# Optimization experiments

Hardware: AMD Instinct MI355X
Metric: run time of the kernel (lower is better)

The kernel has to match this reference:

```python
import jax, jax.numpy as jnp
import numpy as np

NH = 32          # num_attention_heads
LAYER_ID = 3     # per-layer scaling coeff = LAYER_ID + 1
SQ, B, H = 1024, 2, 4096
MEM_LEN = 1024
HD = H // NH


def setup_inputs() -> dict:
    key = jax.random.key(0)
    ks = jax.random.split(key, 6)
    hidden_states = jax.random.normal(ks[0], (SQ, B, H), dtype=jnp.float32)
    mem = jax.random.normal(ks[1], (B, MEM_LEN, 2 * NH * HD), dtype=jnp.float32) * 0.5
    qkv_w = jax.random.normal(ks[2], (3 * H, H), dtype=jnp.float32) * 0.02
    qkv_b = jax.random.normal(ks[3], (3 * H,), dtype=jnp.float32) * 0.02
    dense_w = jax.random.normal(ks[4], (H, H), dtype=jnp.float32) * 0.02
    dense_b = jax.random.normal(ks[5], (H,), dtype=jnp.float32) * 0.02
    # causal mask over new tokens; mem positions fully visible. True = masked.
    kv = MEM_LEN + SQ
    mask = ((jnp.arange(kv)[None, :] - MEM_LEN) > jnp.arange(SQ)[:, None])
    mask = mask[None, None, :, :]  # [1,1,sq,kv]
    # position ids of new tokens continue after the mem cache: [b, sq]
    position_ids = jnp.broadcast_to(MEM_LEN + jnp.arange(SQ, dtype=jnp.int64), (B, SQ))
    return {"hidden_states": hidden_states, "mask": mask, "position_ids": position_ids,
            "mem": mem, "qkv_w": qkv_w, "qkv_b": qkv_b, "dense_w": dense_w, "dense_b": dense_b}


def _rotate_half(x):
    x1, x2 = jnp.split(x, 2, axis=-1)
    return jnp.concatenate((-x2, x1), axis=-1)


def _rotary_tables(max_pos):
    inv_freq = 1.0 / (10000.0 ** (jnp.arange(0, HD, 2, dtype=jnp.float32) / HD))
    t = jnp.arange(max_pos, dtype=jnp.float32)
    freqs = jnp.einsum('i,j->ij', t, inv_freq)          # [L, HD/2]
    emb = jnp.concatenate((freqs, freqs), axis=-1)      # [L, HD]
    return jnp.cos(emb), jnp.sin(emb)


def reference(hidden_states, mask, position_ids, mem, qkv_w, qkv_b, dense_w, dense_b):
    sq, b, h = hidden_states.shape
    coeff = float(LAYER_ID + 1)
    # QKV projection: [sq,b,3H] -> [sq,b,nh,3*hd] -> split
    mixed = jnp.einsum('sbh,oh->sbo', hidden_states, qkv_w) + qkv_b
    mixed = mixed.reshape(sq, b, NH, 3 * HD)
    q, k, v = jnp.split(mixed, 3, axis=-1)              # each [sq,b,nh,hd]
    # rotary embedding with position indices (position_ids: [b,sq] -> [sq,b])
    pos = position_ids.T                                 # [sq,b]
    cos_t, sin_t = _rotary_tables(MEM_LEN + SQ)          # table up to max pos + 1
    cos = cos_t[pos][:, :, None, :]                      # [sq,b,1,hd]
    sin = sin_t[pos][:, :, None, :]
    q = q * cos + _rotate_half(q) * sin
    k = k * cos + _rotate_half(k) * sin
    # mem-KV concat: mem [b, mem_len, 2*nh*hd] -> memk/memv [mem_len,b,nh,hd]
    m = mem.reshape(b, MEM_LEN, 2, NH, HD).transpose(2, 1, 0, 3, 4)
    k = jnp.concatenate((m[0], k), axis=0)               # [kv,b,nh,hd]
    v = jnp.concatenate((m[1], v), axis=0)
    # per-layer scaled attention scores
    q = q / (np.sqrt(HD) * coeff)
    scores = jnp.einsum('sbnh,tbnh->bnst', q, k)         # [b,nh,sq,kv]
    scores = jnp.where(mask, -10000.0, scores)
    scores = scores * coeff
    probs = jax.nn.softmax(scores, axis=-1)
    ctx = jnp.einsum('bnst,tbnh->sbnh', probs, v).reshape(sq, b, h)
    out = jnp.einsum('sbh,oh->sbo', ctx, dense_w) + dense_b
    return out
```

## Files before the change

kernel.cpp:

```cpp
#include <hip/hip_runtime.h>


typedef __attribute__((ext_vector_type(4))) float f32x4;
typedef __attribute__((ext_vector_type(8))) short bf16x8;
typedef unsigned short u16;

#define SQ   1024
#define BSZ  2
#define H    4096
#define NH   32
#define HD   128
#define MEML 1024
#define KV   2048

__device__ __forceinline__ u16 f32_to_bf16(float f) {
  union { float f; unsigned int u; } v; v.f = f;
  unsigned int r = v.u + 0x7FFFu + ((v.u >> 16) & 1u);
  return (u16)(r >> 16);
}
__device__ __forceinline__ float bf16_to_f32(u16 x) {
  union { unsigned int u; float f; } v; v.u = ((unsigned int)x) << 16; return v.f;
}

__device__ __forceinline__ void gload_lds16(const void* g, void* l) {
  __builtin_amdgcn_global_load_lds((const __attribute__((address_space(1))) void*)g,
                                   (__attribute__((address_space(3))) void*)l, 16, 0, 0);
}

__global__ __launch_bounds__(256) void conv_bf16(const float* __restrict__ in,
                                                 u16* __restrict__ out, int n4) {
  int idx = blockIdx.x * 256 + threadIdx.x;
  if (idx < n4) {
    float4 v = ((const float4*)in)[idx];
    ushort4 o;
    o.x = f32_to_bf16(v.x); o.y = f32_to_bf16(v.y);
    o.z = f32_to_bf16(v.z); o.w = f32_to_bf16(v.w);
    ((ushort4*)out)[idx] = o;
  }
}

__global__ __launch_bounds__(256) void rope_tables(float* __restrict__ cost, float* __restrict__ sint) {
  int idx = blockIdx.x * 256 + threadIdx.x;
  int s = idx >> 6, j = idx & 63;
  float inv = powf(10000.0f, -(float)j / 64.0f);
  float ang = (float)(MEML + s) * inv;
  cost[idx] = cosf(ang);
  sint[idx] = sinf(ang);
}

__global__ __launch_bounds__(512, 2) void gemm3p(const u16* __restrict__ A, const u16* __restrict__ B,
                                                 const float* __restrict__ bias, u16* __restrict__ C,
                                                 int N, int K) {
  __shared__ char lds[2][57344];
  const int tid = threadIdx.x;
  const int lane = tid & 63;
  const int w = tid >> 6;
  const int wm = w >> 2, wn = w & 3;
  const int rl = lane & 15, cg = lane >> 4;
  const int m0 = blockIdx.y * 256, n0 = blockIdx.x * 192;
  const int nt = K >> 6;

  const int srow = tid >> 3;
  const int scb = ((tid & 7) << 4) ^ ((srow & 7) << 4);

  auto stage_a = [&](int tile, int ua) {
    if (tile >= nt) return;
    gload_lds16((const char*)(A + (size_t)(m0 + ua * 64 + srow) * K + (size_t)tile * 64) + scb,
                lds[tile & 1] + ua * 8192 + tid * 16);
  };
  auto stage_b = [&](int tile, int ub) {
    if (tile >= nt) return;
    gload_lds16((const char*)(B + (size_t)(n0 + ub * 64 + srow) * K + (size_t)tile * 64) + scb,
                lds[tile & 1] + 32768 + ub * 8192 + tid * 16);
  };

  f32x4 acc[8][3];
#pragma unroll
  for (int i = 0; i < 8; ++i)
#pragma unroll
    for (int j = 0; j < 3; ++j) acc[i][j] = (f32x4){0.f, 0.f, 0.f, 0.f};

  bf16x8 af0[4][2], af1[4][2], bf[3][2];

  auto read_am = [&](const char* buf, int mh, bf16x8 (&dst)[4][2]) {
#pragma unroll
    for (int mi = 0; mi < 4; ++mi) {
      int R = wm * 128 + mh * 64 + mi * 16 + rl;
#pragma unroll
      for (int kk = 0; kk < 2; ++kk) {
        int cb = (kk * 64 + cg * 16) ^ ((R & 7) << 4);
        dst[mi][kk] = *(const bf16x8*)(buf + R * 128 + cb);
      }
    }
  };
  auto read_b1 = [&](const char* buf, int nl) {
    int R = wn * 48 + nl * 16 + rl;
#pragma unroll
    for (int kk = 0; kk < 2; ++kk) {
      int cb = (kk * 64 + cg * 16) ^ ((R & 7) << 4);
      bf[nl][kk] = *(const bf16x8*)(buf + 32768 + R * 128 + cb);
    }
  };

#pragma unroll
  for (int u = 0; u < 4; ++u) stage_a(0, u);
#pragma unroll
  for (int u = 0; u < 3; ++u) stage_b(0, u);
#pragma unroll
  for (int u = 0; u < 3; ++u) stage_b(1, u);
  asm volatile("s_waitcnt vmcnt(3)" ::: "memory");
  __builtin_amdgcn_s_barrier();

  for (int kt = 0; kt < nt; ++kt) {
    const char* buf = lds[kt & 1];
    read_am(buf, 0, af0);
    read_b1(buf, 0); read_b1(buf, 1);
    stage_a(kt + 1, 0); stage_a(kt + 1, 1);
    __builtin_amdgcn_s_barrier();
    asm volatile("s_waitcnt lgkmcnt(0)" ::: "memory");
    __builtin_amdgcn_s_setprio(1);
#pragma unroll
    for (int kk = 0; kk < 2; ++kk)
#pragma unroll
      for (int mi = 0; mi < 4; ++mi) {
        acc[mi][0] = __builtin_amdgcn_mfma_f32_16x16x32_bf16(af0[mi][kk], bf[0][kk], acc[mi][0], 0, 0, 0);
        acc[mi][1] = __builtin_amdgcn_mfma_f32_16x16x32_bf16(af0[mi][kk], bf[1][kk], acc[mi][1], 0, 0, 0);
      }
    __builtin_amdgcn_s_setprio(0);
    __builtin_amdgcn_s_barrier();
    read_am(buf, 1, af1);
    read_b1(buf, 2);
    stage_a(kt + 1, 2); stage_a(kt + 1, 3);
    __builtin_amdgcn_s_barrier();
    asm volatile("s_waitcnt lgkmcnt(0)" ::: "memory");
    __builtin_amdgcn_s_setprio(1);
#pragma unroll
    for (int kk = 0; kk < 2; ++kk)
#pragma unroll
      for (int mi = 0; mi < 4; ++mi) {
        acc[4 + mi][1] = __builtin_amdgcn_mfma_f32_16x16x32_bf16(af1[mi][kk], bf[1][kk], acc[4 + mi][1], 0, 0, 0);
        acc[4 + mi][2] = __builtin_amdgcn_mfma_f32_16x16x32_bf16(af1[mi][kk], bf[2][kk], acc[4 + mi][2], 0, 0, 0);
      }
    __builtin_amdgcn_s_setprio(0);
    __builtin_amdgcn_s_barrier();
    stage_b(kt + 2, 0); stage_b(kt + 2, 1); stage_b(kt + 2, 2);
    __builtin_amdgcn_s_barrier();
    __builtin_amdgcn_s_setprio(1);
#pragma unroll
    for (int kk = 0; kk < 2; ++kk)
#pragma unroll
      for (int mi = 0; mi < 4; ++mi) {
        acc[mi][2] = __builtin_amdgcn_mfma_f32_16x16x32_bf16(af0[mi][kk], bf[2][kk], acc[mi][2], 0, 0, 0);
        acc[4 + mi][0] = __builtin_amdgcn_mfma_f32_16x16x32_bf16(af1[mi][kk], bf[0][kk], acc[4 + mi][0], 0, 0, 0);
      }
    __builtin_amdgcn_s_setprio(0);
    if (kt + 2 < nt)      { asm volatile("s_waitcnt vmcnt(3)" ::: "memory"); }
    else if (kt + 1 < nt) { asm volatile("s_waitcnt vmcnt(0)" ::: "memory"); }
    __builtin_amdgcn_s_barrier();
  }

#pragma unroll
  for (int ni = 0; ni < 3; ++ni) {
    int col = n0 + wn * 48 + ni * 16 + rl;
    float bv = bias[col];
#pragma unroll
    for (int mi = 0; mi < 8; ++mi) {
      int rbase = m0 + wm * 128 + mi * 16 + cg * 4;
#pragma unroll
      for (int j = 0; j < 4; ++j)
        C[(size_t)(rbase + j) * N + col] = f32_to_bf16(acc[mi][ni][j] + bv);
    }
  }
}

__global__ __launch_bounds__(512, 2) void gemm2p(const u16* __restrict__ A, const u16* __restrict__ B,
                                                 const float* __restrict__ bias, float* __restrict__ C,
                                                 int N, int K) {
  __shared__ char lds[2][49152];
  const int tid = threadIdx.x;
  const int lane = tid & 63;
  const int w = tid >> 6;
  const int wm = w >> 2, wn = w & 3;
  const int rl = lane & 15, cg = lane >> 4;
  const int m0 = blockIdx.y * 256, n0 = blockIdx.x * 128;
  const int nt = K >> 6;

  const int srow = tid >> 3;
  const int scb = ((tid & 7) << 4) ^ ((srow & 7) << 4);

  auto stage_a = [&](int tile, int ua) {
    if (tile >= nt) return;
    gload_lds16((const char*)(A + (size_t)(m0 + ua * 64 + srow) * K + (size_t)tile * 64) + scb,
                lds[tile & 1] + ua * 8192 + tid * 16);
  };
  auto stage_b = [&](int tile, int ub) {
    if (tile >= nt) return;
    gload_lds16((const char*)(B + (size_t)(n0 + ub * 64 + srow) * K + (size_t)tile * 64) + scb,
                lds[tile & 1] + 32768 + ub * 8192 + tid * 16);
  };

  f32x4 acc[8][2];
#pragma unroll
  for (int i = 0; i < 8; ++i)
#pragma unroll
    for (int j = 0; j < 2; ++j) acc[i][j] = (f32x4){0.f, 0.f, 0.f, 0.f};

  bf16x8 af0[4][2], af1[4][2], bf[2][2];

  auto read_am = [&](const char* buf, int mh, bf16x8 (&dst)[4][2]) {
#pragma unroll
    for (int mi = 0; mi < 4; ++mi) {
      int R = wm * 128 + mh * 64 + mi * 16 + rl;
#pragma unroll
      for (int kk = 0; kk < 2; ++kk) {
        int cb = (kk * 64 + cg * 16) ^ ((R & 7) << 4);
        dst[mi][kk] = *(const bf16x8*)(buf + R * 128 + cb);
      }
    }
  };
  auto read_b1 = [&](const char* buf, int nl) {
    int R = wn * 32 + nl * 16 + rl;
#pragma unroll
    for (int kk = 0; kk < 2; ++kk) {
      int cb = (kk * 64 + cg * 16) ^ ((R & 7) << 4);
      bf[nl][kk] = *(const bf16x8*)(buf + 32768 + R * 128 + cb);
    }
  };

#pragma unroll
  for (int u = 0; u < 4; ++u) stage_a(0, u);
  stage_b(0, 0); stage_b(0, 1);
  stage_b(1, 0); stage_b(1, 1);
  asm volatile("s_waitcnt vmcnt(2)" ::: "memory");
  __builtin_amdgcn_s_barrier();

  for (int kt = 0; kt < nt; ++kt) {
    const char* buf = lds[kt & 1];
    read_am(buf, 0, af0);
    read_b1(buf, 0); read_b1(buf, 1);
    stage_a(kt + 1, 0); stage_a(kt + 1, 1);
    __builtin_amdgcn_s_barrier();
    asm volatile("s_waitcnt lgkmcnt(0)" ::: "memory");
    __builtin_amdgcn_s_setprio(1);
#pragma unroll
    for (int kk = 0; kk < 2; ++kk)
#pragma unroll
      for (int mi = 0; mi < 4; ++mi) {
        acc[mi][0] = __builtin_amdgcn_mfma_f32_16x16x32_bf16(af0[mi][kk], bf[0][kk], acc[mi][0], 0, 0, 0);
        acc[mi][1] = __builtin_amdgcn_mfma_f32_16x16x32_bf16(af0[mi][kk], bf[1][kk], acc[mi][1], 0, 0, 0);
      }
    __builtin_amdgcn_s_setprio(0);
    __builtin_amdgcn_s_barrier();
    read_am(buf, 1, af1);
    stage_a(kt + 1, 2); stage_a(kt + 1, 3);
    stage_b(kt + 2, 0); stage_b(kt + 2, 1);
    __builtin_amdgcn_s_barrier();
    asm volatile("s_waitcnt lgkmcnt(0)" ::: "memory");
    __builtin_amdgcn_s_setprio(1);
#pragma unroll
    for (int kk = 0; kk < 2; ++kk)
#pragma unroll
      for (int mi = 0; mi < 4; ++mi) {
        acc[4 + mi][0] = __builtin_amdgcn_mfma_f32_16x16x32_bf16(af1[mi][kk], bf[0][kk], acc[4 + mi][0], 0, 0, 0);
        acc[4 + mi][1] = __builtin_amdgcn_mfma_f32_16x16x32_bf16(af1[mi][kk], bf[1][kk], acc[4 + mi][1], 0, 0, 0);
      }
    __builtin_amdgcn_s_setprio(0);
    if (kt + 2 < nt)      { asm volatile("s_waitcnt vmcnt(2)" ::: "memory"); }
    else if (kt + 1 < nt) { asm volatile("s_waitcnt vmcnt(0)" ::: "memory"); }
    __builtin_amdgcn_s_barrier();
  }

#pragma unroll
  for (int ni = 0; ni < 2; ++ni) {
    int col = n0 + wn * 32 + ni * 16 + rl;
    float bv = bias[col];
#pragma unroll
    for (int mi = 0; mi < 8; ++mi) {
      int rbase = m0 + wm * 128 + mi * 16 + cg * 4;
#pragma unroll
      for (int j = 0; j < 4; ++j)
        C[(size_t)(rbase + j) * N + col] = acc[mi][ni][j] + bv;
    }
  }
}

__global__ __launch_bounds__(256) void prep_qk(const u16* __restrict__ mixed,
                                               const float* __restrict__ cost,
                                               const float* __restrict__ sint,
                                               u16* __restrict__ Qb, u16* __restrict__ Kb) {
  int s0 = blockIdx.x * 64, head = blockIdx.y;
  int b = head >> 5, nh = head & 31;
  int tid = threadIdx.x;
  const float qs = 0.08838834764831845f;
#pragma unroll
  for (int i = 0; i < 16; ++i) {
    int flat = i * 256 + tid;
    int sl = flat >> 6, j = flat & 63;
    int s = s0 + sl;
    size_t base = ((size_t)(s * 2 + b)) * 12288 + (size_t)nh * 384;
    float q1 = bf16_to_f32(mixed[base + j]),       q2 = bf16_to_f32(mixed[base + j + 64]);
    float k1 = bf16_to_f32(mixed[base + 128 + j]), k2 = bf16_to_f32(mixed[base + 192 + j]);
    float c = cost[s * 64 + j], sn = sint[s * 64 + j];
    float q1r = q1 * c - q2 * sn, q2r = q2 * c + q1 * sn;
    float k1r = k1 * c - k2 * sn, k2r = k2 * c + k1 * sn;
    size_t qoff = ((size_t)head * SQ + s) * HD;
    Qb[qoff + j]      = f32_to_bf16(q1r * qs);
    Qb[qoff + j + 64] = f32_to_bf16(q2r * qs);
    size_t koff = ((size_t)head * KV + MEML + s) * HD;
    Kb[koff + j]      = f32_to_bf16(k1r);
    Kb[koff + j + 64] = f32_to_bf16(k2r);
  }
}

__global__ __launch_bounds__(256) void prep_kv(const u16* __restrict__ mixed,
                                               const float* __restrict__ mem,
                                               u16* __restrict__ Kb, u16* __restrict__ Vtb) {
  int t0 = blockIdx.x * 64, head = blockIdx.y;
  int b = head >> 5, nh = head & 31;
  __shared__ u16 vt[128 * 72];
  int tid = threadIdx.x;
  if (t0 < MEML) {
#pragma unroll
    for (int i = 0; i < 32; ++i) {
      int flat = i * 256 + tid;
      int tl = flat >> 7, d = flat & 127;
      float kvv = mem[((size_t)b * MEML + t0 + tl) * 8192 + (size_t)nh * HD + d];
      Kb[((size_t)head * KV + t0 + tl) * HD + d] = f32_to_bf16(kvv);
    }
  }
#pragma unroll
  for (int i = 0; i < 32; ++i) {
    int flat = i * 256 + tid;
    int tl = flat >> 7, d = flat & 127;
    int t = t0 + tl;
    u16 v;
    if (t < MEML) v = f32_to_bf16(mem[((size_t)b * MEML + t) * 8192 + 4096 + (size_t)nh * HD + d]);
    else          v = mixed[((size_t)((t - MEML) * 2 + b)) * 12288 + (size_t)nh * 384 + 256 + d];
    vt[d * 72 + tl] = v;
  }
  __syncthreads();
#pragma unroll
  for (int i = 0; i < 4; ++i) {
    int c = i * 256 + tid;
    int d = c >> 3, slot = c & 7;
    *(bf16x8*)(Vtb + ((size_t)head * HD + d) * KV + t0 + slot * 8) =
        *(const bf16x8*)(vt + d * 72 + slot * 8);
  }
}

__global__ __launch_bounds__(512) void attn_fwd(const u16* __restrict__ Qb, const u16* __restrict__ Kb,
                                                const u16* __restrict__ Vtb, u16* __restrict__ ctx) {
  __shared__ u16 Ks[2][64 * 128];
  __shared__ u16 Vts[2][128 * 64];
  __shared__ u16 Ps[8 * 16 * 64];
  const int tid = threadIdx.x;
  const int lane = tid & 63;
  const int w = tid >> 6;
  const int q0 = blockIdx.x * 128;
  const int head = blockIdx.y;
  const int rl = lane & 15, cg = lane >> 4;

  bf16x8 qf[4];
  {
    const u16* Qrow = Qb + ((size_t)head * SQ + q0 + w * 16 + rl) * HD;
#pragma unroll
    for (int kk = 0; kk < 4; ++kk)
      qf[kk] = *(const bf16x8*)(Qrow + kk * 32 + cg * 8);
  }

  f32x4 acc[8];
#pragma unroll
  for (int i = 0; i < 8; ++i) acc[i] = (f32x4){0.f, 0.f, 0.f, 0.f};
  float mrow[4] = {-3.0e38f, -3.0e38f, -3.0e38f, -3.0e38f};
  float lrow[4] = {0.f, 0.f, 0.f, 0.f};

  const int ntile = (MEML + q0 + 128) >> 6;

  auto stageKV = [&](int it) {
    int t0 = it * 64;
    int buf = it & 1;
#pragma unroll
    for (int i = 0; i < 2; ++i) {
      int flat = i * 512 + tid;
      int row = flat >> 4;
      int scb = ((flat & 15) << 4) ^ ((row & 7) << 4);
      gload_lds16((const char*)(Kb + ((size_t)head * KV + t0 + row) * HD) + scb,
                  (char*)Ks[buf] + (flat << 4));
    }
#pragma unroll
    for (int i = 0; i < 2; ++i) {
      int flat = i * 512 + tid;
      int row = flat >> 3;
      int scb = ((flat & 7) << 4) ^ ((row & 7) << 4);
      gload_lds16((const char*)(Vtb + ((size_t)head * HD + row) * KV + t0) + scb,
                  (char*)Vts[buf] + (flat << 4));
    }
  };

  stageKV(0);

  for (int it = 0; it < ntile; ++it) {
    const int t0 = it * 64;
    if (it + 1 < ntile) {
      stageKV(it + 1);
      asm volatile("s_waitcnt vmcnt(4)" ::: "memory");
    } else {
      asm volatile("s_waitcnt vmcnt(0)" ::: "memory");
    }
    __builtin_amdgcn_s_barrier();
    const char* Kbuf = (const char*)Ks[it & 1];
    const char* Vbuf = (const char*)Vts[it & 1];
    const bool live = (t0 - MEML) <= (q0 + w * 16 + 15);
    if (live) {
      f32x4 sf[4];
#pragma unroll
      for (int tn = 0; tn < 4; ++tn) {
        f32x4 s = (f32x4){0.f, 0.f, 0.f, 0.f};
#pragma unroll
        for (int kk = 0; kk < 4; ++kk) {
          int row = tn * 16 + rl;
          int cb = (kk * 64 + cg * 16) ^ ((row & 7) << 4);
          bf16x8 kf = *(const bf16x8*)(Kbuf + row * 256 + cb);
          s = __builtin_amdgcn_mfma_f32_16x16x32_bf16(qf[kk], kf, s, 0, 0, 0);
        }
        sf[tn] = s;
      }
      if (t0 + 63 > MEML + q0 + w * 16) {
#pragma unroll
        for (int tn = 0; tn < 4; ++tn)
#pragma unroll
          for (int j = 0; j < 4; ++j) {
            int t = t0 + tn * 16 + rl;
            int srowq = q0 + w * 16 + cg * 4 + j;
            if (t - MEML > srowq) sf[tn][j] = -40000.0f;
          }
      }
      float mt[4];
#pragma unroll
      for (int j = 0; j < 4; ++j)
        mt[j] = fmaxf(fmaxf(sf[0][j], sf[1][j]), fmaxf(sf[2][j], sf[3][j]));
#pragma unroll
      for (int off = 1; off <= 8; off <<= 1)
#pragma unroll
        for (int j = 0; j < 4; ++j) mt[j] = fmaxf(mt[j], __shfl_xor(mt[j], off, 64));
      float pscale[4];
#pragma unroll
      for (int j = 0; j < 4; ++j) {
        float mn = fmaxf(mrow[j], mt[j]);
        pscale[j] = __expf(mrow[j] - mn);
        mrow[j] = mn;
      }
      float lsum[4] = {0.f, 0.f, 0.f, 0.f};
#pragma unroll
      for (int tn = 0; tn < 4; ++tn)
#pragma unroll
        for (int j = 0; j < 4; ++j) {
          float p = __expf(sf[tn][j] - mrow[j]);
          lsum[j] += p;
          int prow = cg * 4 + j;
          int colb = (tn * 16 + rl) * 2;
          int addr = w * 2048 + prow * 128 + (colb ^ ((prow & 7) << 4));
          *(u16*)((char*)Ps + addr) = f32_to_bf16(p);
        }
#pragma unroll
      for (int off = 1; off <= 8; off <<= 1)
#pragma unroll
        for (int j = 0; j < 4; ++j) lsum[j] += __shfl_xor(lsum[j], off, 64);
#pragma unroll
      for (int j = 0; j < 4; ++j) lrow[j] = lrow[j] * pscale[j] + lsum[j];
#pragma unroll
      for (int dn = 0; dn < 8; ++dn)
#pragma unroll
        for (int j = 0; j < 4; ++j) acc[dn][j] *= pscale[j];
#pragma unroll
      for (int dn = 0; dn < 8; ++dn) {
#pragma unroll
        for (int kk2 = 0; kk2 < 2; ++kk2) {
          int pcb = (kk2 * 64 + cg * 16) ^ ((rl & 7) << 4);
          bf16x8 pf = *(const bf16x8*)((const char*)Ps + w * 2048 + rl * 128 + pcb);
          int vrow = dn * 16 + rl;
          int vcb = (kk2 * 64 + cg * 16) ^ ((vrow & 7) << 4);
          bf16x8 vf = *(const bf16x8*)(Vbuf + vrow * 128 + vcb);
          acc[dn] = __builtin_amdgcn_mfma_f32_16x16x32_bf16(pf, vf, acc[dn], 0, 0, 0);
        }
      }
    }
    __builtin_amdgcn_s_barrier();
  }

  const int b = head >> 5, nh = head & 31;
#pragma unroll
  for (int dn = 0; dn < 8; ++dn)
#pragma unroll
    for (int j = 0; j < 4; ++j) {
      int srowq = q0 + w * 16 + cg * 4 + j;
      float v = acc[dn][j] / lrow[j];
      ctx[((size_t)(srowq * 2 + b)) * H + (size_t)nh * HD + dn * 16 + rl] = f32_to_bf16(v);
    }
}

extern "C" void kernel_launch(void* const* d_in, const int* in_sizes, int n_in,
                              void* d_out, int out_size, void* d_ws, size_t ws_size,
                              hipStream_t stream) {
  const float* hidden  = (const float*)d_in[0];
  const float* mem     = (const float*)d_in[3];
  const float* qkv_w   = (const float*)d_in[4];
  const float* qkv_b   = (const float*)d_in[5];
  const float* dense_w = (const float*)d_in[6];
  const float* dense_b = (const float*)d_in[7];
  float* out = (float*)d_out;
  char* ws = (char*)d_ws;

  u16* mixed = (u16*)ws;
  char* R1 = ws + 100663296;
  u16* hid_bf = (u16*)R1;
  u16* qw_bf  = (u16*)(R1 + 16777216);
  u16* Qb  = (u16*)R1;
  u16* Kb  = (u16*)(R1 + 16777216);
  u16* Vtb = (u16*)(R1 + 50331648);
  u16* ctx = (u16*)(R1 + 83886080);
  u16* dw_bf = (u16*)(R1 + 100663296);
  float* cost = (float*)(ws + 234881024);
  float* sint = (float*)(ws + 234881024 + 262144);

  conv_bf16<<<8192, 256, 0, stream>>>(hidden, hid_bf, 2097152);
  conv_bf16<<<49152, 256, 0, stream>>>(qkv_w, qw_bf, 12582912);
  rope_tables<<<256, 256, 0, stream>>>(cost, sint);
  gemm3p<<<dim3(64, 8), 512, 0, stream>>>(hid_bf, qw_bf, qkv_b, mixed, 12288, 4096);
  prep_qk<<<dim3(16, 64), 256, 0, stream>>>(mixed, cost, sint, Qb, Kb);
  prep_kv<<<dim3(32, 64), 256, 0, stream>>>(mixed, mem, Kb, Vtb);
  conv_bf16<<<16384, 256, 0, stream>>>(dense_w, dw_bf, 4194304);
  attn_fwd<<<dim3(8, 64), 512, 0, stream>>>(Qb, Kb, Vtb, ctx);
  gemm2p<<<dim3(32, 8), 512, 0, stream>>>(ctx, dw_bf, dense_b, out, 4096, 4096);
}
```

Baseline: 571.2 us.

## Fuse fp32-to-bf16 weight conversion into GEMM B-tile staging

Drops the separate conversion kernels for qkv_w and dense_w. Both GEMMs now load fp32 weight tiles into registers two tiles ahead, convert them to bf16, and write them into swizzled LDS, in place of direct global-to-LDS loads of pre-converted bf16. This removes the extra read/write pass over roughly 200MB of weights. In exchange, weight bytes fetched by the GEMMs double, redundant conversion is repeated across the 8 M-blocks, register pressure rises, and a full vmcnt(0) wait each iteration may reduce load/compute overlap.

```diff
diff --git a/kernel.cpp b/kernel.cpp
--- a/kernel.cpp
+++ b/kernel.cpp
@@ -48,7 +48,7 @@
   sint[idx] = sinf(ang);
 }
 
-__global__ __launch_bounds__(512, 2) void gemm3p(const u16* __restrict__ A, const u16* __restrict__ B,
+__global__ __launch_bounds__(512, 2) void gemm3p(const u16* __restrict__ A, const float* __restrict__ Bf,
                                                  const float* __restrict__ bias, u16* __restrict__ C,
                                                  int N, int K) {
   __shared__ char lds[2][57344];
@@ -61,17 +61,21 @@
   const int nt = K >> 6;
 
   const int srow = tid >> 3;
-  const int scb = ((tid & 7) << 4) ^ ((srow & 7) << 4);
+  const int cB = tid & 7;
+  const int scb = (cB << 4) ^ ((srow & 7) << 4);
 
   auto stage_a = [&](int tile, int ua) {
     if (tile >= nt) return;
     gload_lds16((const char*)(A + (size_t)(m0 + ua * 64 + srow) * K + (size_t)tile * 64) + scb,
                 lds[tile & 1] + ua * 8192 + tid * 16);
   };
-  auto stage_b = [&](int tile, int ub) {
-    if (tile >= nt) return;
-    gload_lds16((const char*)(B + (size_t)(n0 + ub * 64 + srow) * K + (size_t)tile * 64) + scb,
-                lds[tile & 1] + 32768 + ub * 8192 + tid * 16);
+  auto wrB = [&](char* bufb, int u, float4 lo, float4 hi) {
+    union { bf16x8 v; u16 e[8]; } pk;
+    pk.e[0] = f32_to_bf16(lo.x); pk.e[1] = f32_to_bf16(lo.y);
+    pk.e[2] = f32_to_bf16(lo.z); pk.e[3] = f32_to_bf16(lo.w);
+    pk.e[4] = f32_to_bf16(hi.x); pk.e[5] = f32_to_bf16(hi.y);
+    pk.e[6] = f32_to_bf16(hi.z); pk.e[7] = f32_to_bf16(hi.w);
+    *(bf16x8*)(bufb + 32768 + u * 8192 + srow * 128 + ((cB << 4) ^ ((srow & 7) << 4))) = pk.v;
   };
 
   f32x4 acc[8][3];
@@ -105,14 +109,29 @@
 #pragma unroll
   for (int u = 0; u < 4; ++u) stage_a(0, u);
 #pragma unroll
-  for (int u = 0; u < 3; ++u) stage_b(0, u);
-#pragma unroll
-  for (int u = 0; u < 3; ++u) stage_b(1, u);
-  asm volatile("s_waitcnt vmcnt(3)" ::: "memory");
+  for (int t = 0; t < 2; ++t)
+#pragma unroll
+    for (int u = 0; u < 3; ++u) {
+      const float* s = Bf + (size_t)(n0 + u * 64 + srow) * K + (size_t)t * 64 + cB * 8;
+      float4 lo = ((const float4*)s)[0];
+      float4 hi = ((const float4*)s)[1];
+      wrB(lds[t], u, lo, hi);
+    }
+  asm volatile("s_waitcnt vmcnt(0) lgkmcnt(0)" ::: "memory");
   __builtin_amdgcn_s_barrier();
 
   for (int kt = 0; kt < nt; ++kt) {
-    const char* buf = lds[kt & 1];
+    char* buf = lds[kt & 1];
+    const bool pf = (kt + 2 < nt);
+    float4 rb[6];
+    if (pf) {
+#pragma unroll
+      for (int u = 0; u < 3; ++u) {
+        const float* s = Bf + (size_t)(n0 + u * 64 + srow) * K + (size_t)(kt + 2) * 64 + cB * 8;
+        rb[u * 2]     = ((const float4*)s)[0];
+        rb[u * 2 + 1] = ((const float4*)s)[1];
+      }
+    }
     read_am(buf, 0, af0);
     read_b1(buf, 0); read_b1(buf, 1);
     stage_a(kt + 1, 0); stage_a(kt + 1, 1);
@@ -143,7 +162,11 @@
       }
     __builtin_amdgcn_s_setprio(0);
     __builtin_amdgcn_s_barrier();
-    stage_b(kt + 2, 0); stage_b(kt + 2, 1); stage_b(kt + 2, 2);
+    if (pf) {
+#pragma unroll
+      for (int u = 0; u < 3; ++u) wrB(buf, u, rb[u * 2], rb[u * 2 + 1]);
+    }
+    asm volatile("s_waitcnt lgkmcnt(0)" ::: "memory");
     __builtin_amdgcn_s_barrier();
     __builtin_amdgcn_s_setprio(1);
 #pragma unroll
@@ -154,8 +177,7 @@
         acc[4 + mi][0] = __builtin_amdgcn_mfma_f32_16x16x32_bf16(af1[mi][kk], bf[0][kk], acc[4 + mi][0], 0, 0, 0);
       }
     __builtin_amdgcn_s_setprio(0);
-    if (kt + 2 < nt)      { asm volatile("s_waitcnt vmcnt(3)" ::: "memory"); }
-    else if (kt + 1 < nt) { asm volatile("s_waitcnt vmcnt(0)" ::: "memory"); }
+    asm volatile("s_waitcnt vmcnt(0)" ::: "memory");
     __builtin_amdgcn_s_barrier();
   }
 
@@ -173,7 +195,7 @@
   }
 }
 
-__global__ __launch_bounds__(512, 2) void gemm2p(const u16* __restrict__ A, const u16* __restrict__ B,
+__global__ __launch_bounds__(512, 2) void gemm2p(const u16* __restrict__ A, const float* __restrict__ Bf,
                                                  const float* __restrict__ bias, float* __restrict__ C,
                                                  int N, int K) {
   __shared__ char lds[2][49152];
@@ -186,17 +208,21 @@
   const int nt = K >> 6;
 
   const int srow = tid >> 3;
-  const int scb = ((tid & 7) << 4) ^ ((srow & 7) << 4);
+  const int cB = tid & 7;
+  const int scb = (cB << 4) ^ ((srow & 7) << 4);
 
   auto stage_a = [&](int tile, int ua) {
     if (tile >= nt) return;
     gload_lds16((const char*)(A + (size_t)(m0 + ua * 64 + srow) * K + (size_t)tile * 64) + scb,
                 lds[tile & 1] + ua * 8192 + tid * 16);
   };
-  auto stage_b = [&](int tile, int ub) {
-    if (tile >= nt) return;
-    gload_lds16((const char*)(B + (size_t)(n0 + ub * 64 + srow) * K + (size_t)tile * 64) + scb,
-                lds[tile & 1] + 32768 + ub * 8192 + tid * 16);
+  auto wrB = [&](char* bufb, int u, float4 lo, float4 hi) {
+    union { bf16x8 v; u16 e[8]; } pk;
+    pk.e[0] = f32_to_bf16(lo.x); pk.e[1] = f32_to_bf16(lo.y);
+    pk.e[2] = f32_to_bf16(lo.z); pk.e[3] = f32_to_bf16(lo.w);
+    pk.e[4] = f32_to_bf16(hi.x); pk.e[5] = f32_to_bf16(hi.y);
+    pk.e[6] = f32_to_bf16(hi.z); pk.e[7] = f32_to_bf16(hi.w);
+    *(bf16x8*)(bufb + 32768 + u * 8192 + srow * 128 + ((cB << 4) ^ ((srow & 7) << 4))) = pk.v;
   };
 
   f32x4 acc[8][2];
@@ -229,13 +255,30 @@
 
 #pragma unroll
   for (int u = 0; u < 4; ++u) stage_a(0, u);
-  stage_b(0, 0); stage_b(0, 1);
-  stage_b(1, 0); stage_b(1, 1);
-  asm volatile("s_waitcnt vmcnt(2)" ::: "memory");
+#pragma unroll
+  for (int t = 0; t < 2; ++t)
+#pragma unroll
+    for (int u = 0; u < 2; ++u) {
+      const float* s = Bf + (size_t)(n0 + u * 64 + srow) * K + (size_t)t * 64 + cB * 8;
+      float4 lo = ((const float4*)s)[0];
+      float4 hi = ((const float4*)s)[1];
+      wrB(lds[t], u, lo, hi);
+    }
+  asm volatile("s_waitcnt vmcnt(0) lgkmcnt(0)" ::: "memory");
   __builtin_amdgcn_s_barrier();
 
   for (int kt = 0; kt < nt; ++kt) {
-    const char* buf = lds[kt & 1];
+    char* buf = lds[kt & 1];
+    const bool pf = (kt + 2 < nt);
+    float4 rb[4];
+    if (pf) {
+#pragma unroll
+      for (int u = 0; u < 2; ++u) {
+        const float* s = Bf + (size_t)(n0 + u * 64 + srow) * K + (size_t)(kt + 2) * 64 + cB * 8;
+        rb[u * 2]     = ((const float4*)s)[0];
+        rb[u * 2 + 1] = ((const float4*)s)[1];
+      }
+    }
     read_am(buf, 0, af0);
     read_b1(buf, 0); read_b1(buf, 1);
     stage_a(kt + 1, 0); stage_a(kt + 1, 1);
@@ -253,7 +296,7 @@
     __builtin_amdgcn_s_barrier();
     read_am(buf, 1, af1);
     stage_a(kt + 1, 2); stage_a(kt + 1, 3);
-    stage_b(kt + 2, 0); stage_b(kt + 2, 1);
+    if (pf) { wrB(buf, 0, rb[0], rb[1]); wrB(buf, 1, rb[2], rb[3]); }
     __builtin_amdgcn_s_barrier();
     asm volatile("s_waitcnt lgkmcnt(0)" ::: "memory");
     __builtin_amdgcn_s_setprio(1);
@@ -265,8 +308,7 @@
         acc[4 + mi][1] = __builtin_amdgcn_mfma_f32_16x16x32_bf16(af1[mi][kk], bf[1][kk], acc[4 + mi][1], 0, 0, 0);
       }
     __builtin_amdgcn_s_setprio(0);
-    if (kt + 2 < nt)      { asm volatile("s_waitcnt vmcnt(2)" ::: "memory"); }
-    else if (kt + 1 < nt) { asm volatile("s_waitcnt vmcnt(0)" ::: "memory"); }
+    asm volatile("s_waitcnt vmcnt(0)" ::: "memory");
     __builtin_amdgcn_s_barrier();
   }
 
@@ -514,22 +556,18 @@
   u16* mixed = (u16*)ws;
   char* R1 = ws + 100663296;
   u16* hid_bf = (u16*)R1;
-  u16* qw_bf  = (u16*)(R1 + 16777216);
   u16* Qb  = (u16*)R1;
   u16* Kb  = (u16*)(R1 + 16777216);
   u16* Vtb = (u16*)(R1 + 50331648);
   u16* ctx = (u16*)(R1 + 83886080);
-  u16* dw_bf = (u16*)(R1 + 100663296);
   float* cost = (float*)(ws + 234881024);
   float* sint = (float*)(ws + 234881024 + 262144);
 
   conv_bf16<<<8192, 256, 0, stream>>>(hidden, hid_bf, 2097152);
-  conv_bf16<<<49152, 256, 0, stream>>>(qkv_w, qw_bf, 12582912);
   rope_tables<<<256, 256, 0, stream>>>(cost, sint);
-  gemm3p<<<dim3(64, 8), 512, 0, stream>>>(hid_bf, qw_bf, qkv_b, mixed, 12288, 4096);
+  gemm3p<<<dim3(64, 8), 512, 0, stream>>>(hid_bf, qkv_w, qkv_b, mixed, 12288, 4096);
   prep_qk<<<dim3(16, 64), 256, 0, stream>>>(mixed, cost, sint, Qb, Kb);
   prep_kv<<<dim3(32, 64), 256, 0, stream>>>(mixed, mem, Kb, Vtb);
-  conv_bf16<<<16384, 256, 0, stream>>>(dense_w, dw_bf, 4194304);
   attn_fwd<<<dim3(8, 64), 512, 0, stream>>>(Qb, Kb, Vtb, ctx);
-  gemm2p<<<dim3(32, 8), 512, 0, stream>>>(ctx, dw_bf, dense_b, out, 4096, 4096);
-}
+  gemm2p<<<dim3(32, 8), 512, 0, stream>>>(ctx, dense_w, dense_b, out, 4096, 4096);
+}
```

After: 621.7 us. 1.09x slower.
